# Kernel tuning notes

Hardware: AMD Instinct MI355X
Metric: run time of the kernel (lower is better)

Reference implementation:

```python
import jax, jax.numpy as jnp
import numpy as np

PAD = 1
VOCAB, D, HOPS = 32000, 256, 3

def _gru_dir(x_tbd, h0, Wih, Whh, bih, bhh):
    # x_tbd: [T,B,D]; PyTorch GRU gate math
    def step(h, xt):
        gx = xt @ Wih.T + bih            # [B,3D]
        gh = h @ Whh.T + bhh
        xr, xz, xn = jnp.split(gx, 3, axis=-1)
        hr, hz, hn = jnp.split(gh, 3, axis=-1)
        r = jax.nn.sigmoid(xr + hr)
        z = jax.nn.sigmoid(xz + hz)
        n = jnp.tanh(xn + r * hn)
        h2 = (1.0 - z) * n + z * h
        return h2, h2
    hT, ys = jax.lax.scan(step, h0, x_tbd)
    return ys, hT

def _embed_bag(table, idx):
    # idx: [B,L,M] -> sum over M -> [B,L,D]
    return jnp.take(table, idx, axis=0).sum(axis=2)

def _add_lm(full_mem, kb_len, conv_len, hiddens):
    # full_mem: [B,L,D]; hiddens: [B,T,D]; write hiddens into rows [kb, kb+cl)
    B, L, _ = full_mem.shape
    T = hiddens.shape[1]
    pos = jnp.arange(L)[None, :]                      # [1,L]
    rel = pos - kb_len[:, None]                        # [B,L]
    valid = (rel >= 0) & (rel < conv_len[:, None])
    rel_c = jnp.clip(rel, 0, T - 1)
    gathered = jnp.take_along_axis(hiddens, rel_c[:, :, None], axis=1)  # [B,L,D]
    return full_mem + jnp.where(valid[:, :, None], gathered, 0.0)

def setup_inputs() -> dict:
    key = jax.random.key(0)
    ks = jax.random.split(key, 20)
    B, T, L, M = 32, 128, 512, 4
    conv_seqs = jax.random.randint(ks[0], (B, T, M), 0, VOCAB)
    src_seqs = jax.random.randint(ks[1], (B, L, M), 0, VOCAB)
    kb_len = jnp.full((B,), L - T, dtype=jnp.int32)
    conv_len = jnp.full((B,), T, dtype=jnp.int32)
    def zero_pad(t):
        return t.at[PAD].set(0.0)
    emb_ctx = zero_pad(0.1 * jax.random.normal(ks[2], (VOCAB, D)))
    C_tables = zero_pad(0.1 * jax.random.normal(ks[3], (HOPS + 1, VOCAB, D)).transpose(1, 0, 2)).transpose(1, 0, 2)
    s = 1.0 / np.sqrt(D)
    Wih_f = jax.random.uniform(ks[4], (3 * D, D), minval=-s, maxval=s)
    Whh_f = jax.random.uniform(ks[5], (3 * D, D), minval=-s, maxval=s)
    bih_f = jax.random.uniform(ks[6], (3 * D,), minval=-s, maxval=s)
    bhh_f = jax.random.uniform(ks[7], (3 * D,), minval=-s, maxval=s)
    Wih_b = jax.random.uniform(ks[8], (3 * D, D), minval=-s, maxval=s)
    Whh_b = jax.random.uniform(ks[9], (3 * D, D), minval=-s, maxval=s)
    bih_b = jax.random.uniform(ks[10], (3 * D,), minval=-s, maxval=s)
    bhh_b = jax.random.uniform(ks[11], (3 * D,), minval=-s, maxval=s)
    W_w = jax.random.uniform(ks[12], (D, 2 * D), minval=-s, maxval=s)
    W_b = jax.random.uniform(ks[13], (D,), minval=-s, maxval=s)
    proj_w = jax.random.uniform(ks[14], (D, 2 * D), minval=-s, maxval=s)
    proj_b = jax.random.uniform(ks[15], (D,), minval=-s, maxval=s)
    return dict(conv_seqs=conv_seqs, src_seqs=src_seqs, kb_len=kb_len, conv_len=conv_len,
                emb_ctx=emb_ctx, C_tables=C_tables,
                Wih_f=Wih_f, Whh_f=Whh_f, bih_f=bih_f, bhh_f=bhh_f,
                Wih_b=Wih_b, Whh_b=Whh_b, bih_b=bih_b, bhh_b=bhh_b,
                W_w=W_w, W_b=W_b, proj_w=proj_w, proj_b=proj_b)

def reference(conv_seqs, src_seqs, kb_len, conv_len, emb_ctx, C_tables,
              Wih_f, Whh_f, bih_f, bhh_f, Wih_b, Whh_b, bih_b, bhh_b,
              W_w, W_b, proj_w, proj_b):
    B = conv_seqs.shape[0]
    # ContextRNN (dropout is identity at eval)
    emb = _embed_bag(emb_ctx, conv_seqs)               # [B,T,D]
    x = emb.transpose(1, 0, 2)                          # [T,B,D]
    h0 = jnp.zeros((B, D), emb.dtype)
    ys_f, hT_f = _gru_dir(x, h0, Wih_f, Whh_f, bih_f, bhh_f)
    ys_b, hT_b = _gru_dir(x[::-1], h0, Wih_b, Whh_b, bih_b, bhh_b)
    outputs = jnp.concatenate([ys_f, ys_b[::-1]], axis=-1).transpose(1, 0, 2)  # [B,T,2D]
    hidden = jnp.concatenate([hT_f, hT_b], axis=-1) @ W_w.T + W_b              # [B,D]
    rnn_out = outputs @ W_w.T + W_b                                            # [B,T,D]
    # ExternalKnowledge encode
    u = hidden
    prob_logit = None
    embed_C = None
    for hop in range(HOPS):
        embed_A = _add_lm(_embed_bag(C_tables[hop], src_seqs), kb_len, conv_len, rnn_out)
        embed_C = _add_lm(_embed_bag(C_tables[hop + 1], src_seqs), kb_len, conv_len, rnn_out)
        prob_logit = jnp.einsum('bld,bd->bl', embed_A, u)
        prob = jax.nn.softmax(prob_logit, axis=1)
        o_k = jnp.einsum('bld,bl->bd', embed_C, prob)
        u = u + o_k
    global_pointer = jax.nn.sigmoid(prob_logit)
    encoded = jax.nn.relu(jnp.concatenate([hidden, u], axis=-1) @ proj_w.T + proj_b)[None]
    return global_pointer, encoded
```

## Files before the change

kernel.cpp:

```cpp
#include <hip/hip_runtime.h>

typedef _Float16 f16;
typedef _Float16 f16x8 __attribute__((ext_vector_type(8)));
typedef _Float16 f16x4 __attribute__((ext_vector_type(4)));
typedef float    f32x4 __attribute__((ext_vector_type(4)));


__device__ __forceinline__ float frcp(float x){
  float r; asm("v_rcp_f32 %0, %1" : "=v"(r) : "v"(x)); return r;
}
__device__ __forceinline__ float fsig(float x){ return frcp(1.0f + __expf(-x)); }
__device__ __forceinline__ float ftanh(float x){ return 2.0f*frcp(1.0f + __expf(-2.0f*x)) - 1.0f; }

__global__ void k_zero(float* out){
  int i = blockIdx.x*256 + threadIdx.x;
  if (i < 24576) out[i] = 0.f;
}

__global__ void k_cvtall(const float* __restrict__ s0, const float* __restrict__ s1,
                         const float* __restrict__ s2, const float* __restrict__ s3,
                         const float* __restrict__ s4,
                         f16* __restrict__ d0, f16* __restrict__ d1,
                         f16* __restrict__ d2, f16* __restrict__ d3,
                         f16* __restrict__ d4){
  int i = blockIdx.x*256 + threadIdx.x;
  d0[i] = (f16)s0[i];
  d1[i] = (f16)s1[i];
  d2[i] = (f16)s2[i];
  d3[i] = (f16)s3[i];
  if (i < 131072) d4[i] = (f16)s4[i];
}

__global__ void k_embbag(const int* __restrict__ conv, const float* __restrict__ tbl,
                         f16* __restrict__ emb){
  int bt = blockIdx.x, d = threadIdx.x;
  const int* ix = conv + (size_t)bt*4;
  float s = 0.f;
#pragma unroll
  for (int m = 0; m < 4; ++m) s += tbl[(size_t)ix[m]*256 + d];
  emb[(size_t)bt*256 + d] = (f16)s;
}

__global__ __launch_bounds__(256) void k_gx(const f16* __restrict__ emb,
                                            const f16* __restrict__ W16,
                                            const float* __restrict__ bih,
                                            const float* __restrict__ bhh,
                                            f16* __restrict__ gx, int rev){
  int lane = threadIdx.x & 63, wv = threadIdx.x >> 6;
  int l16 = lane & 15, l4 = lane >> 4;
  int mrow = blockIdx.x*64 + wv*16;
  int m = mrow + l16;
  int t = m >> 5, b = m & 31;
  int tsrc = rev ? (127 - t) : t;
  const f16* arow = emb + (size_t)(b*128 + tsrc)*256;
  f16x8 af[8];
#pragma unroll
  for (int kt = 0; kt < 8; ++kt) af[kt] = *(const f16x8*)(arow + kt*32 + l4*8);

  for (int nt = 0; nt < 48; ++nt){
    int n = nt*16 + l16;
    const f16* brow = W16 + (size_t)n*256;
    f32x4 acc = {0.f,0.f,0.f,0.f};
#pragma unroll
    for (int kt = 0; kt < 8; ++kt){
      f16x8 bf = *(const f16x8*)(brow + kt*32 + l4*8);
      acc = __builtin_amdgcn_mfma_f32_16x16x32_f16(af[kt], bf, acc, 0, 0, 0);
    }
    float bias = bih[n] + (n < 512 ? bhh[n] : 0.f);
#pragma unroll
    for (int r = 0; r < 4; ++r){
      int m2 = mrow + l4*4 + r;
      gx[(size_t)m2*768 + n] = (f16)(acc[r] + bias);
    }
  }
}

__global__ __launch_bounds__(512, 1) void k_gru(const f16* __restrict__ gx_f,
                                                const f16* __restrict__ gx_b,
                                                const f16* __restrict__ whhf16,
                                                const f16* __restrict__ whhb16,
                                                const float* __restrict__ bhh_f,
                                                const float* __restrict__ bhh_b,
                                                f16* __restrict__ Abuf){
  int dir = blockIdx.x >> 1, grp = blockIdx.x & 1, b0 = grp*16;
  const f16*   gx  = dir ? gx_b   : gx_f;
  const f16*   Whh = dir ? whhb16 : whhf16;
  const float* bhh = dir ? bhh_b  : bhh_f;

  int tid = threadIdx.x, lane = tid & 63, wv = tid >> 6;
  int l16 = lane & 15, l4 = lane >> 4;

  __shared__ __align__(16) f16   a16[2][16][264];
  __shared__ __align__(16) float bhnL[256];
  for (int i = tid; i < (16*264*2)/4; i += 512) ((unsigned*)&a16[0][0][0])[i] = 0u;
  if (tid < 256) bhnL[tid] = bhh[512 + tid];

  f16x8 aW[2][3][8];
#pragma unroll
  for (int q = 0; q < 2; ++q){
    int Q = 2*wv + q;
#pragma unroll
    for (int g = 0; g < 3; ++g){
      const f16* wrow = Whh + (size_t)(g*256 + Q*16 + l16)*256;
#pragma unroll
      for (int kt = 0; kt < 8; ++kt) aW[q][g][kt] = *(const f16x8*)(wrow + kt*32 + l4*8);
    }
  }

  const f16* gp = gx + (size_t)(b0 + l16)*768;
  f16* ap  = Abuf + (size_t)(b0 + l16)*128*512 + dir*256
           + (size_t)(dir ? 127 : 0)*512;
  int  astep = dir ? -512 : 512;
  f16* app = ap;

  const int d00 = (2*wv    )*16 + l4*4;
  const int d01 = (2*wv + 1)*16 + l4*4;

  f16x4 pend[2];
  pend[0] = (f16x4){(f16)0.f,(f16)0.f,(f16)0.f,(f16)0.f};
  pend[1] = (f16x4){(f16)0.f,(f16)0.f,(f16)0.f,(f16)0.f};

  __syncthreads();

#pragma unroll 1
  for (int t = 0; t < 128; ++t){
    if (t){
      *(f16x4*)(app + d00) = pend[0];
      *(f16x4*)(app + d01) = pend[1];
    }

    f16x4 xg[2][3];
#pragma unroll
    for (int q = 0; q < 2; ++q)
#pragma unroll
      for (int g = 0; g < 3; ++g)
        xg[q][g] = *(const f16x4*)(gp + g*256 + (2*wv+q)*16 + l4*4);

    const f16* rb = &a16[t & 1][l16][l4*8];

    f32x4 accr[2], accz[2];
#pragma unroll
    for (int q = 0; q < 2; ++q){ accr[q] = (f32x4){0.f,0.f,0.f,0.f};
                                 accz[q] = (f32x4){0.f,0.f,0.f,0.f}; }
#pragma unroll
    for (int kt = 0; kt < 8; ++kt){
      f16x8 bf = *(const f16x8*)(rb + kt*32);
#pragma unroll
      for (int q = 0; q < 2; ++q){
        accr[q] = __builtin_amdgcn_mfma_f32_16x16x32_f16(aW[q][0][kt], bf, accr[q], 0, 0, 0);
        accz[q] = __builtin_amdgcn_mfma_f32_16x16x32_f16(aW[q][1][kt], bf, accz[q], 0, 0, 0);
      }
    }

    f32x4 accn[2];
#pragma unroll
    for (int q = 0; q < 2; ++q) accn[q] = (f32x4){0.f,0.f,0.f,0.f};
#pragma unroll
    for (int kt = 0; kt < 8; ++kt){
      f16x8 bf = *(const f16x8*)(rb + kt*32);
#pragma unroll
      for (int q = 0; q < 2; ++q)
        accn[q] = __builtin_amdgcn_mfma_f32_16x16x32_f16(aW[q][2][kt], bf, accn[q], 0, 0, 0);
    }

    float rr[2][4], zz[2][4];
#pragma unroll
    for (int q = 0; q < 2; ++q)
#pragma unroll
      for (int r = 0; r < 4; ++r){
        rr[q][r] = fsig((float)xg[q][0][r] + accr[q][r]);
        zz[q][r] = fsig((float)xg[q][1][r] + accz[q][r]);
      }

    int nxt = (t & 1) ^ 1;
#pragma unroll
    for (int q = 0; q < 2; ++q){
      int d0 = (2*wv+q)*16 + l4*4;
      float4 bh4 = *(const float4*)(&bhnL[d0]);
      f16x4 hold = pend[q];
      f16x4 o4;
#pragma unroll
      for (int r = 0; r < 4; ++r){
        float bh = (r==0)?bh4.x:(r==1)?bh4.y:(r==2)?bh4.z:bh4.w;
        float nn = ftanh((float)xg[q][2][r] + rr[q][r]*(accn[q][r] + bh));
        float h2 = nn + zz[q][r]*((float)hold[r] - nn);
        o4[r] = (f16)h2;
      }
      *(f16x4*)(&a16[nxt][l16][d0]) = o4;
      pend[q] = o4;
    }
    app = ap; ap += astep;
    gp += 24576;
    __syncthreads();
  }
  *(f16x4*)(app + d00) = pend[0];
  *(f16x4*)(app + d01) = pend[1];
}

__global__ __launch_bounds__(256) void k_rnnout(const f16* __restrict__ Abuf,
                                                const f16* __restrict__ Ww16,
                                                const float* __restrict__ Wb,
                                                float* __restrict__ rnn){
  int lane = threadIdx.x & 63, wv = threadIdx.x >> 6;
  int l16 = lane & 15, l4 = lane >> 4;
  int mrow = blockIdx.x*64 + wv*16;
  const f16* arow = Abuf + (size_t)(mrow + l16)*512;
  f16x8 af[16];
#pragma unroll
  for (int kt = 0; kt < 16; ++kt) af[kt] = *(const f16x8*)(arow + kt*32 + l4*8);
  for (int nt = 0; nt < 16; ++nt){
    int n = nt*16 + l16;
    const f16* brow = Ww16 + (size_t)n*512;
    f32x4 acc = {0.f,0.f,0.f,0.f};
#pragma unroll
    for (int kt = 0; kt < 16; ++kt){
      f16x8 bf = *(const f16x8*)(brow + kt*32 + l4*8);
      acc = __builtin_amdgcn_mfma_f32_16x16x32_f16(af[kt], bf, acc, 0, 0, 0);
    }
    float bias = Wb[n];
#pragma unroll
    for (int r = 0; r < 4; ++r)
      rnn[(size_t)(mrow + l4*4 + r)*256 + n] = acc[r] + bias;
  }
}

__global__ __launch_bounds__(256) void k_hidden(const f16* __restrict__ Abuf,
                                                const f16* __restrict__ Ww16,
                                                const float* __restrict__ Wb,
                                                float* __restrict__ hidden,
                                                float* __restrict__ u){
  int lane = threadIdx.x & 63, wv = threadIdx.x >> 6;
  int l16 = lane & 15, l4 = lane >> 4;
  int mt = wv & 1, nt = blockIdx.x*2 + (wv >> 1);
  int b = mt*16 + l16;
  const f16* rowf = Abuf + ((size_t)b*128 + 127)*512;
  const f16* rowb = Abuf + ((size_t)b*128)*512;
  f16x8 af[16];
#pragma unroll
  for (int kt = 0; kt < 16; ++kt){
    int k = kt*32 + l4*8;
    af[kt] = *(const f16x8*)((k < 256 ? rowf : rowb) + k);
  }
  int n = nt*16 + l16;
  const f16* brow = Ww16 + (size_t)n*512;
  f32x4 acc = {0.f,0.f,0.f,0.f};
#pragma unroll
  for (int kt = 0; kt < 16; ++kt){
    f16x8 bf = *(const f16x8*)(brow + kt*32 + l4*8);
    acc = __builtin_amdgcn_mfma_f32_16x16x32_f16(af[kt], bf, acc, 0, 0, 0);
  }
  float bias = Wb[n];
#pragma unroll
  for (int r = 0; r < 4; ++r){
    int bo = mt*16 + l4*4 + r;
    float v = acc[r] + bias;
    hidden[(size_t)bo*256 + n] = v;
    u[(size_t)bo*256 + n] = v;
  }
}

__global__ __launch_bounds__(256) void k_logits(const int* __restrict__ src,
                                                const int* __restrict__ kbl,
                                                const int* __restrict__ cvl,
                                                const float* __restrict__ tblA,
                                                const float* __restrict__ rnn,
                                                const float* __restrict__ u,
                                                float* __restrict__ logits){
  int b = blockIdx.x >> 5, chunk = blockIdx.x & 31;
  int lane = threadIdx.x & 63, wv = threadIdx.x >> 6;
  int kb = kbl[b], cl = cvl[b];
  float4 uv = *(const float4*)(u + b*256 + lane*4);
#pragma unroll
  for (int i = 0; i < 4; ++i){
    int l = chunk*16 + wv*4 + i;
    const int* sp = src + ((size_t)b*512 + l)*4;
    float b0 = 0.f, b1 = 0.f, b2 = 0.f, b3 = 0.f;
#pragma unroll
    for (int m = 0; m < 4; ++m){
      float4 wq = *(const float4*)(tblA + (size_t)sp[m]*256 + lane*4);
      b0 += wq.x; b1 += wq.y; b2 += wq.z; b3 += wq.w;
    }
    int rel = l - kb;
    if (rel >= 0 && rel < cl){
      int rc = rel < 127 ? rel : 127;
      float4 rv = *(const float4*)(rnn + ((size_t)b*128 + rc)*256 + lane*4);
      b0 += rv.x; b1 += rv.y; b2 += rv.z; b3 += rv.w;
    }
    float p = b0*uv.x + b1*uv.y + b2*uv.z + b3*uv.w;
#pragma unroll
    for (int off = 32; off >= 1; off >>= 1) p += __shfl_down(p, off);
    if (lane == 0) logits[(size_t)b*512 + l] = p;
  }
}

__global__ __launch_bounds__(256) void k_okv(const int* __restrict__ src,
                                             const int* __restrict__ kbl,
                                             const int* __restrict__ cvl,
                                             const float* __restrict__ tblC,
                                             const float* __restrict__ rnn,
                                             const float* __restrict__ logits,
                                             float* __restrict__ u,
                                             float* __restrict__ gp_out, int write_gp){
  int b = blockIdx.x >> 3, c = blockIdx.x & 7;
  int d = threadIdx.x, lane = d & 63, wv = d >> 6;
  __shared__ float red[4];
  __shared__ float bc;
  __shared__ float pr[512];
  __shared__ int   sidx[256];

  float v0 = logits[(size_t)b*512 + d];
  float v1 = logits[(size_t)b*512 + 256 + d];
  float m = fmaxf(v0, v1);
#pragma unroll
  for (int off = 32; off >= 1; off >>= 1) m = fmaxf(m, __shfl_down(m, off));
  if (lane == 0) red[wv] = m;
  __syncthreads();
  if (d == 0) bc = fmaxf(fmaxf(red[0], red[1]), fmaxf(red[2], red[3]));
  __syncthreads();
  float mx = bc;
  float e0 = __expf(v0 - mx), e1 = __expf(v1 - mx);
  float s = e0 + e1;
#pragma unroll
  for (int off = 32; off >= 1; off >>= 1) s += __shfl_down(s, off);
  __syncthreads();
  if (lane == 0) red[wv] = s;
  __syncthreads();
  if (d == 0) bc = red[0] + red[1] + red[2] + red[3];
  __syncthreads();
  float inv = 1.0f/bc;
  pr[d] = e0*inv; pr[256 + d] = e1*inv;
  sidx[d] = src[(size_t)b*2048 + c*256 + d];
  if (write_gp && c == 0){
    gp_out[(size_t)b*512 + d]       = fsig(v0);
    gp_out[(size_t)b*512 + 256 + d] = fsig(v1);
  }
  __syncthreads();

  int kb = kbl[b], cl = cvl[b];
  float acc = 0.f;
  for (int l = 0; l < 64; ++l){
    const int* sp = sidx + l*4;
    float bag = tblC[(size_t)sp[0]*256 + d] + tblC[(size_t)sp[1]*256 + d]
              + tblC[(size_t)sp[2]*256 + d] + tblC[(size_t)sp[3]*256 + d];
    int rel = (c*64 + l) - kb;
    if (rel >= 0 && rel < cl){
      int rc = rel < 127 ? rel : 127;
      bag += rnn[((size_t)b*128 + rc)*256 + d];
    }
    acc += pr[c*64 + l] * bag;
  }
  atomicAdd(&u[(size_t)b*256 + d], acc);
}

__global__ void k_encoded(const float* __restrict__ hidden, const float* __restrict__ u,
                          const float* __restrict__ pw, const float* __restrict__ pb,
                          float* __restrict__ out){
  int b = blockIdx.x, d = threadIdx.x;
  const float* w = pw + (size_t)d*512;
  float s = pb[d];
  for (int k = 0; k < 256; ++k) s += hidden[b*256 + k] * w[k];
  for (int k = 0; k < 256; ++k) s += u[b*256 + k]      * w[256 + k];
  out[(size_t)b*256 + d] = fmaxf(s, 0.f);
}

extern "C" void kernel_launch(void* const* d_in, const int* in_sizes, int n_in,
                              void* d_out, int out_size, void* d_ws, size_t ws_size,
                              hipStream_t stream){
  (void)in_sizes; (void)n_in; (void)out_size;
  float* out = (float*)d_out;

  const size_t WS_NEEDED = 25034752;
  if (ws_size < WS_NEEDED){
    k_zero<<<96, 256, 0, stream>>>(out);
    return;
  }

  const int* conv  = (const int*)d_in[0];
  const int* src   = (const int*)d_in[1];
  const int* kbl   = (const int*)d_in[2];
  const int* cvl   = (const int*)d_in[3];
  const float* emb_ctx = (const float*)d_in[4];
  const float* Ct      = (const float*)d_in[5];
  const float* Wih_f = (const float*)d_in[6];
  const float* Whh_f = (const float*)d_in[7];
  const float* bih_f = (const float*)d_in[8];
  const float* bhh_f = (const float*)d_in[9];
  const float* Wih_b = (const float*)d_in[10];
  const float* Whh_b = (const float*)d_in[11];
  const float* bih_b = (const float*)d_in[12];
  const float* bhh_b = (const float*)d_in[13];
  const float* Ww = (const float*)d_in[14];
  const float* Wb = (const float*)d_in[15];
  const float* pw = (const float*)d_in[16];
  const float* pb = (const float*)d_in[17];

  char* ws = (char*)d_ws;
  f16*   emb    = (f16*)(ws);
  f16*   gx_f   = (f16*)(ws + 2097152);
  f16*   gx_b   = (f16*)(ws + 8388608);
  f16*   Abuf   = (f16*)(ws + 14680064);
  float* rnn    = (float*)(ws + 18874368);
  float* hidden = (float*)(ws + 23068672);
  float* u      = (float*)(ws + 23101440);
  float* logits = (float*)(ws + 23134208);
  f16*   wihf16 = (f16*)(ws + 23199744);
  f16*   wihb16 = (f16*)(ws + 23592960);
  f16*   whhf16 = (f16*)(ws + 23986176);
  f16*   whhb16 = (f16*)(ws + 24379392);
  f16*   ww16   = (f16*)(ws + 24772608);

  k_cvtall<<<768, 256, 0, stream>>>(Wih_f, Wih_b, Whh_f, Whh_b, Ww,
                                    wihf16, wihb16, whhf16, whhb16, ww16);
  k_embbag<<<4096, 256, 0, stream>>>(conv, emb_ctx, emb);
  k_gx<<<64, 256, 0, stream>>>(emb, wihf16, bih_f, bhh_f, gx_f, 0);
  k_gx<<<64, 256, 0, stream>>>(emb, wihb16, bih_b, bhh_b, gx_b, 1);
  k_gru<<<4, 512, 0, stream>>>(gx_f, gx_b, whhf16, whhb16, bhh_f, bhh_b, Abuf);
  k_rnnout<<<64, 256, 0, stream>>>(Abuf, ww16, Wb, rnn);
  k_hidden<<<8, 256, 0, stream>>>(Abuf, ww16, Wb, hidden, u);

  for (int hop = 0; hop < 3; ++hop){
    const float* tA = Ct + (size_t)hop     * 32000 * 256;
    const float* tC = Ct + (size_t)(hop+1) * 32000 * 256;
    k_logits<<<1024, 256, 0, stream>>>(src, kbl, cvl, tA, rnn, u, logits);
    k_okv<<<256, 256, 0, stream>>>(src, kbl, cvl, tC, rnn, logits, u,
                                   out, hop == 2 ? 1 : 0);
  }
  k_encoded<<<32, 256, 0, stream>>>(hidden, u, pw, pb, out + 16384);
}
```

Baseline: 916.2 us.

## Split GRU recurrence across 16 waves, one hidden tile per wave

The recurrent GRU kernel now launches 1024 threads per block instead of 512, and each wave owns a single 16-column hidden tile instead of two. This halves the serial MFMA chain and gate math per wave on each time step, shortening the latency-bound critical path of the 128-step recurrence. In exchange the per-step block barrier covers twice as many waves, and per-wave weight registers drop from 48 to 24 vectors. The gx loads for the n gate are also deferred until after the r/z MFMAs.

```diff
diff --git a/kernel.cpp b/kernel.cpp
--- a/kernel.cpp
+++ b/kernel.cpp
@@ -75,13 +75,13 @@
   }
 }
 
-__global__ __launch_bounds__(512, 1) void k_gru(const f16* __restrict__ gx_f,
-                                                const f16* __restrict__ gx_b,
-                                                const f16* __restrict__ whhf16,
-                                                const f16* __restrict__ whhb16,
-                                                const float* __restrict__ bhh_f,
-                                                const float* __restrict__ bhh_b,
-                                                f16* __restrict__ Abuf){
+__global__ __launch_bounds__(1024, 1) void k_gru(const f16* __restrict__ gx_f,
+                                                 const f16* __restrict__ gx_b,
+                                                 const f16* __restrict__ whhf16,
+                                                 const f16* __restrict__ whhb16,
+                                                 const float* __restrict__ bhh_f,
+                                                 const float* __restrict__ bhh_b,
+                                                 f16* __restrict__ Abuf){
   int dir = blockIdx.x >> 1, grp = blockIdx.x & 1, b0 = grp*16;
   const f16*   gx  = dir ? gx_b   : gx_f;
   const f16*   Whh = dir ? whhb16 : whhf16;
@@ -92,109 +92,80 @@
 
   __shared__ __align__(16) f16   a16[2][16][264];
   __shared__ __align__(16) float bhnL[256];
-  for (int i = tid; i < (16*264*2)/4; i += 512) ((unsigned*)&a16[0][0][0])[i] = 0u;
+  for (int i = tid; i < (16*264*2)/4; i += 1024) ((unsigned*)&a16[0][0][0])[i] = 0u;
   if (tid < 256) bhnL[tid] = bhh[512 + tid];
 
-  f16x8 aW[2][3][8];
-#pragma unroll
-  for (int q = 0; q < 2; ++q){
-    int Q = 2*wv + q;
-#pragma unroll
-    for (int g = 0; g < 3; ++g){
-      const f16* wrow = Whh + (size_t)(g*256 + Q*16 + l16)*256;
-#pragma unroll
-      for (int kt = 0; kt < 8; ++kt) aW[q][g][kt] = *(const f16x8*)(wrow + kt*32 + l4*8);
-    }
-  }
-
+  const int Q = wv;
+  f16x8 aW[3][8];
+#pragma unroll
+  for (int g = 0; g < 3; ++g){
+    const f16* wrow = Whh + (size_t)(g*256 + Q*16 + l16)*256;
+#pragma unroll
+    for (int kt = 0; kt < 8; ++kt) aW[g][kt] = *(const f16x8*)(wrow + kt*32 + l4*8);
+  }
+
+  const int d0 = Q*16 + l4*4;
   const f16* gp = gx + (size_t)(b0 + l16)*768;
   f16* ap  = Abuf + (size_t)(b0 + l16)*128*512 + dir*256
            + (size_t)(dir ? 127 : 0)*512;
   int  astep = dir ? -512 : 512;
   f16* app = ap;
 
-  const int d00 = (2*wv    )*16 + l4*4;
-  const int d01 = (2*wv + 1)*16 + l4*4;
-
-  f16x4 pend[2];
-  pend[0] = (f16x4){(f16)0.f,(f16)0.f,(f16)0.f,(f16)0.f};
-  pend[1] = (f16x4){(f16)0.f,(f16)0.f,(f16)0.f,(f16)0.f};
+  f16x4 pend = (f16x4){(f16)0.f,(f16)0.f,(f16)0.f,(f16)0.f};
 
   __syncthreads();
 
 #pragma unroll 1
   for (int t = 0; t < 128; ++t){
-    if (t){
-      *(f16x4*)(app + d00) = pend[0];
-      *(f16x4*)(app + d01) = pend[1];
-    }
-
-    f16x4 xg[2][3];
-#pragma unroll
-    for (int q = 0; q < 2; ++q)
-#pragma unroll
-      for (int g = 0; g < 3; ++g)
-        xg[q][g] = *(const f16x4*)(gp + g*256 + (2*wv+q)*16 + l4*4);
+    if (t) *(f16x4*)(app + d0) = pend;
+
+    f16x4 xgr = *(const f16x4*)(gp + 0*256 + d0);
+    f16x4 xgz = *(const f16x4*)(gp + 1*256 + d0);
 
     const f16* rb = &a16[t & 1][l16][l4*8];
 
-    f32x4 accr[2], accz[2];
-#pragma unroll
-    for (int q = 0; q < 2; ++q){ accr[q] = (f32x4){0.f,0.f,0.f,0.f};
-                                 accz[q] = (f32x4){0.f,0.f,0.f,0.f}; }
+    f32x4 accr = {0.f,0.f,0.f,0.f}, accz = {0.f,0.f,0.f,0.f};
 #pragma unroll
     for (int kt = 0; kt < 8; ++kt){
       f16x8 bf = *(const f16x8*)(rb + kt*32);
-#pragma unroll
-      for (int q = 0; q < 2; ++q){
-        accr[q] = __builtin_amdgcn_mfma_f32_16x16x32_f16(aW[q][0][kt], bf, accr[q], 0, 0, 0);
-        accz[q] = __builtin_amdgcn_mfma_f32_16x16x32_f16(aW[q][1][kt], bf, accz[q], 0, 0, 0);
-      }
-    }
-
-    f32x4 accn[2];
-#pragma unroll
-    for (int q = 0; q < 2; ++q) accn[q] = (f32x4){0.f,0.f,0.f,0.f};
+      accr = __builtin_amdgcn_mfma_f32_16x16x32_f16(aW[0][kt], bf, accr, 0, 0, 0);
+      accz = __builtin_amdgcn_mfma_f32_16x16x32_f16(aW[1][kt], bf, accz, 0, 0, 0);
+    }
+
+    f16x4 xgn = *(const f16x4*)(gp + 2*256 + d0);
+    f32x4 accn = {0.f,0.f,0.f,0.f};
 #pragma unroll
     for (int kt = 0; kt < 8; ++kt){
       f16x8 bf = *(const f16x8*)(rb + kt*32);
-#pragma unroll
-      for (int q = 0; q < 2; ++q)
-        accn[q] = __builtin_amdgcn_mfma_f32_16x16x32_f16(aW[q][2][kt], bf, accn[q], 0, 0, 0);
-    }
-
-    float rr[2][4], zz[2][4];
-#pragma unroll
-    for (int q = 0; q < 2; ++q)
-#pragma unroll
-      for (int r = 0; r < 4; ++r){
-        rr[q][r] = fsig((float)xg[q][0][r] + accr[q][r]);
-        zz[q][r] = fsig((float)xg[q][1][r] + accz[q][r]);
-      }
+      accn = __builtin_amdgcn_mfma_f32_16x16x32_f16(aW[2][kt], bf, accn, 0, 0, 0);
+    }
+
+    float rr[4], zz[4];
+#pragma unroll
+    for (int r = 0; r < 4; ++r){
+      rr[r] = fsig((float)xgr[r] + accr[r]);
+      zz[r] = fsig((float)xgz[r] + accz[r]);
+    }
 
     int nxt = (t & 1) ^ 1;
-#pragma unroll
-    for (int q = 0; q < 2; ++q){
-      int d0 = (2*wv+q)*16 + l4*4;
-      float4 bh4 = *(const float4*)(&bhnL[d0]);
-      f16x4 hold = pend[q];
-      f16x4 o4;
-#pragma unroll
-      for (int r = 0; r < 4; ++r){
-        float bh = (r==0)?bh4.x:(r==1)?bh4.y:(r==2)?bh4.z:bh4.w;
-        float nn = ftanh((float)xg[q][2][r] + rr[q][r]*(accn[q][r] + bh));
-        float h2 = nn + zz[q][r]*((float)hold[r] - nn);
-        o4[r] = (f16)h2;
-      }
-      *(f16x4*)(&a16[nxt][l16][d0]) = o4;
-      pend[q] = o4;
-    }
+    float4 bh4 = *(const float4*)(&bhnL[d0]);
+    f16x4 hold = pend;
+    f16x4 o4;
+#pragma unroll
+    for (int r = 0; r < 4; ++r){
+      float bh = (r==0)?bh4.x:(r==1)?bh4.y:(r==2)?bh4.z:bh4.w;
+      float nn = ftanh((float)xgn[r] + rr[r]*(accn[r] + bh));
+      float h2 = nn + zz[r]*((float)hold[r] - nn);
+      o4[r] = (f16)h2;
+    }
+    *(f16x4*)(&a16[nxt][l16][d0]) = o4;
+    pend = o4;
+
     app = ap; ap += astep;
     gp += 24576;
     __syncthreads();
   }
-  *(f16x4*)(app + d00) = pend[0];
-  *(f16x4*)(app + d01) = pend[1];
+  *(f16x4*)(app + d0) = pend;
 }
 
 __global__ __launch_bounds__(256) void k_rnnout(const f16* __restrict__ Abuf,
@@ -414,7 +385,7 @@
   k_embbag<<<4096, 256, 0, stream>>>(conv, emb_ctx, emb);
   k_gx<<<64, 256, 0, stream>>>(emb, wihf16, bih_f, bhh_f, gx_f, 0);
   k_gx<<<64, 256, 0, stream>>>(emb, wihb16, bih_b, bhh_b, gx_b, 1);
-  k_gru<<<4, 512, 0, stream>>>(gx_f, gx_b, whhf16, whhb16, bhh_f, bhh_b, Abuf);
+  k_gru<<<4, 1024, 0, stream>>>(gx_f, gx_b, whhf16, whhb16, bhh_f, bhh_b, Abuf);
   k_rnnout<<<64, 256, 0, stream>>>(Abuf, ww16, Wb, rnn);
   k_hidden<<<8, 256, 0, stream>>>(Abuf, ww16, Wb, hidden, u);
 
```

Measured after the change: 941.6 us. 2.8% more time.

## Split GRU recurrence across two cooperating blocks with global-memory flag exchange

Applied to the files above, without the earlier changes.

Adds a k_gru_duo kernel that splits each (direction, batch-group) GRU recurrence across two workgroups, each computing half the hidden units. After every timestep the two halves swap their half of the hidden state through global memory, using per-step release/acquire flags tagged with an epoch counter that k_cvtall increments. This halves per-CU MFMA and register work on the serial critical path but adds a cross-CU handshake each step. It relies on the workspace being large enough and on both partner blocks being co-resident, otherwise it falls back to the old kernel.

```diff
diff --git a/kernel.cpp b/kernel.cpp
--- a/kernel.cpp
+++ b/kernel.cpp
@@ -4,6 +4,7 @@
 typedef _Float16 f16x8 __attribute__((ext_vector_type(8)));
 typedef _Float16 f16x4 __attribute__((ext_vector_type(4)));
 typedef float    f32x4 __attribute__((ext_vector_type(4)));
+typedef unsigned long long u64;
 
 
 __device__ __forceinline__ float frcp(float x){
@@ -22,8 +23,9 @@
                          const float* __restrict__ s4,
                          f16* __restrict__ d0, f16* __restrict__ d1,
                          f16* __restrict__ d2, f16* __restrict__ d3,
-                         f16* __restrict__ d4){
+                         f16* __restrict__ d4, unsigned* epoch){
   int i = blockIdx.x*256 + threadIdx.x;
+  if (epoch && i == 0) atomicAdd(epoch, 1u);
   d0[i] = (f16)s0[i];
   d1[i] = (f16)s1[i];
   d2[i] = (f16)s2[i];
@@ -75,13 +77,13 @@
   }
 }
 
-__global__ __launch_bounds__(512, 1) void k_gru(const f16* __restrict__ gx_f,
-                                                const f16* __restrict__ gx_b,
-                                                const f16* __restrict__ whhf16,
-                                                const f16* __restrict__ whhb16,
-                                                const float* __restrict__ bhh_f,
-                                                const float* __restrict__ bhh_b,
-                                                f16* __restrict__ Abuf){
+__global__ __launch_bounds__(512, 1) void k_gru_solo(const f16* __restrict__ gx_f,
+                                                     const f16* __restrict__ gx_b,
+                                                     const f16* __restrict__ whhf16,
+                                                     const f16* __restrict__ whhb16,
+                                                     const float* __restrict__ bhh_f,
+                                                     const float* __restrict__ bhh_b,
+                                                     f16* __restrict__ Abuf){
   int dir = blockIdx.x >> 1, grp = blockIdx.x & 1, b0 = grp*16;
   const f16*   gx  = dir ? gx_b   : gx_f;
   const f16*   Whh = dir ? whhb16 : whhf16;
@@ -108,8 +110,7 @@
   }
 
   const f16* gp = gx + (size_t)(b0 + l16)*768;
-  f16* ap  = Abuf + (size_t)(b0 + l16)*128*512 + dir*256
-           + (size_t)(dir ? 127 : 0)*512;
+  f16* ap  = Abuf + (size_t)(b0 + l16)*128*512 + dir*256 + (size_t)(dir ? 127 : 0)*512;
   int  astep = dir ? -512 : 512;
   f16* app = ap;
 
@@ -128,7 +129,6 @@
       *(f16x4*)(app + d00) = pend[0];
       *(f16x4*)(app + d01) = pend[1];
     }
-
     f16x4 xg[2][3];
 #pragma unroll
     for (int q = 0; q < 2; ++q)
@@ -151,7 +151,6 @@
         accz[q] = __builtin_amdgcn_mfma_f32_16x16x32_f16(aW[q][1][kt], bf, accz[q], 0, 0, 0);
       }
     }
-
     f32x4 accn[2];
 #pragma unroll
     for (int q = 0; q < 2; ++q) accn[q] = (f32x4){0.f,0.f,0.f,0.f};
@@ -162,7 +161,6 @@
       for (int q = 0; q < 2; ++q)
         accn[q] = __builtin_amdgcn_mfma_f32_16x16x32_f16(aW[q][2][kt], bf, accn[q], 0, 0, 0);
     }
-
     float rr[2][4], zz[2][4];
 #pragma unroll
     for (int q = 0; q < 2; ++q)
@@ -171,7 +169,6 @@
         rr[q][r] = fsig((float)xg[q][0][r] + accr[q][r]);
         zz[q][r] = fsig((float)xg[q][1][r] + accz[q][r]);
       }
-
     int nxt = (t & 1) ^ 1;
 #pragma unroll
     for (int q = 0; q < 2; ++q){
@@ -195,6 +192,128 @@
   }
   *(f16x4*)(app + d00) = pend[0];
   *(f16x4*)(app + d01) = pend[1];
+}
+
+__global__ __launch_bounds__(512, 1) void k_gru_duo(const f16* __restrict__ gx_f,
+                                                    const f16* __restrict__ gx_b,
+                                                    const f16* __restrict__ whhf16,
+                                                    const f16* __restrict__ whhb16,
+                                                    const float* __restrict__ bhh_f,
+                                                    const float* __restrict__ bhh_b,
+                                                    f16* __restrict__ Abuf,
+                                                    char* __restrict__ ext){
+  int bid = blockIdx.x;
+  int dir = bid >> 2, grp = (bid >> 1) & 1, half = bid & 1;
+  int b0 = grp*16;
+  const f16*   gx  = dir ? gx_b   : gx_f;
+  const f16*   Whh = dir ? whhb16 : whhf16;
+  const float* bhh = dir ? bhh_b  : bhh_f;
+
+  int tid = threadIdx.x, lane = tid & 63, wv = tid >> 6;
+  int l16 = lane & 15, l4 = lane >> 4;
+
+  __shared__ __align__(16) f16   a16[2][16][264];
+  __shared__ __align__(16) float bhnL[256];
+  for (int i = tid; i < (16*264*2)/4; i += 512) ((unsigned*)&a16[0][0][0])[i] = 0u;
+  if (tid < 256) bhnL[tid] = bhh[512 + tid];
+
+  int pair = dir*2 + grp;
+  char*     hx_mine    = ext + (size_t)((pair*2 + half      )*2)*4096;
+  char*     hx_partner = ext + (size_t)((pair*2 + (half^1))*2)*4096;
+  unsigned* flags_mine    = (unsigned*)(ext + 131072) + (pair*2 + half      )*128;
+  unsigned* flags_partner = (unsigned*)(ext + 131072) + (pair*2 + (half^1))*128;
+  unsigned epoch = __hip_atomic_load((unsigned*)(ext + 135168),
+                                     __ATOMIC_RELAXED, __HIP_MEMORY_SCOPE_AGENT);
+
+  const int Qg = half*8 + wv;
+  const int d0 = Qg*16 + l4*4;
+  f16x8 aW[3][8];
+#pragma unroll
+  for (int g = 0; g < 3; ++g){
+    const f16* wrow = Whh + (size_t)(g*256 + Qg*16 + l16)*256;
+#pragma unroll
+    for (int kt = 0; kt < 8; ++kt) aW[g][kt] = *(const f16x8*)(wrow + kt*32 + l4*8);
+  }
+
+  const f16* gp = gx + (size_t)(b0 + l16)*768;
+  f16* ap  = Abuf + (size_t)(b0 + l16)*128*512 + dir*256 + (size_t)(dir ? 127 : 0)*512;
+  int  astep = dir ? -512 : 512;
+  f16* app = ap;
+
+  const int myoff = l16*256 + wv*32 + l4*8;
+  const int cb = tid >> 5;
+  const int cc = (tid & 31) * 4;
+  const int poff = (half^1)*128;
+
+  f16x4 pend = (f16x4){(f16)0.f,(f16)0.f,(f16)0.f,(f16)0.f};
+
+  __syncthreads();
+
+#pragma unroll 1
+  for (int t = 0; t < 128; ++t){
+    if (t) *(f16x4*)(app + d0) = pend;
+
+    const f16* rb = &a16[t & 1][l16][l4*8];
+    f16x8 bf[8];
+#pragma unroll
+    for (int kt = 0; kt < 8; ++kt) bf[kt] = *(const f16x8*)(rb + kt*32);
+
+    f16x4 xgr = *(const f16x4*)(gp + 0*256 + d0);
+    f16x4 xgz = *(const f16x4*)(gp + 1*256 + d0);
+    f16x4 xgn = *(const f16x4*)(gp + 2*256 + d0);
+
+    f32x4 accr = {0.f,0.f,0.f,0.f}, accz = {0.f,0.f,0.f,0.f};
+#pragma unroll
+    for (int kt = 0; kt < 8; ++kt){
+      accr = __builtin_amdgcn_mfma_f32_16x16x32_f16(aW[0][kt], bf[kt], accr, 0, 0, 0);
+      accz = __builtin_amdgcn_mfma_f32_16x16x32_f16(aW[1][kt], bf[kt], accz, 0, 0, 0);
+    }
+    f32x4 accn = {0.f,0.f,0.f,0.f};
+#pragma unroll
+    for (int kt = 0; kt < 8; ++kt)
+      accn = __builtin_amdgcn_mfma_f32_16x16x32_f16(aW[2][kt], bf[kt], accn, 0, 0, 0);
+
+    float rr[4], zz[4];
+#pragma unroll
+    for (int r = 0; r < 4; ++r){
+      rr[r] = fsig((float)xgr[r] + accr[r]);
+      zz[r] = fsig((float)xgz[r] + accz[r]);
+    }
+
+    int nxt = (t & 1) ^ 1;
+    float4 bh4 = *(const float4*)(&bhnL[d0]);
+    f16x4 hold = pend;
+    f16x4 o4;
+#pragma unroll
+    for (int r = 0; r < 4; ++r){
+      float bh = (r==0)?bh4.x:(r==1)?bh4.y:(r==2)?bh4.z:bh4.w;
+      float nn = ftanh((float)xgn[r] + rr[r]*(accn[r] + bh));
+      float h2 = nn + zz[r]*((float)hold[r] - nn);
+      o4[r] = (f16)h2;
+    }
+    *(f16x4*)(&a16[nxt][l16][d0]) = o4;
+    pend = o4;
+    app = ap; ap += astep;
+    gp += 24576;
+
+    if (t < 127){
+      __hip_atomic_store((u64*)(hx_mine + (size_t)(t&1)*4096 + myoff),
+                         __builtin_bit_cast(u64, o4),
+                         __ATOMIC_RELAXED, __HIP_MEMORY_SCOPE_AGENT);
+      __syncthreads();
+      if (tid == 0)
+        __hip_atomic_store(&flags_mine[t], epoch,
+                           __ATOMIC_RELEASE, __HIP_MEMORY_SCOPE_AGENT);
+      while (__hip_atomic_load(&flags_partner[t],
+                               __ATOMIC_ACQUIRE, __HIP_MEMORY_SCOPE_AGENT) != epoch)
+        __builtin_amdgcn_s_sleep(2);
+      u64 v = __hip_atomic_load((u64*)(hx_partner + (size_t)(t&1)*4096 + cb*256 + cc*2),
+                                __ATOMIC_RELAXED, __HIP_MEMORY_SCOPE_AGENT);
+      *(u64*)((char*)&a16[nxt][cb][0] + (size_t)(poff + cc)*2) = v;
+      __syncthreads();
+    }
+  }
+  *(f16x4*)(app + d0) = pend;
 }
 
 __global__ __launch_bounds__(256) void k_rnnout(const f16* __restrict__ Abuf,
@@ -370,10 +489,13 @@
   float* out = (float*)d_out;
 
   const size_t WS_NEEDED = 25034752;
+  const size_t EXT_OFF   = 25034752;
+  const size_t WS_BIG    = EXT_OFF + 135176;
   if (ws_size < WS_NEEDED){
     k_zero<<<96, 256, 0, stream>>>(out);
     return;
   }
+  bool big = ws_size >= WS_BIG;
 
   const int* conv  = (const int*)d_in[0];
   const int* src   = (const int*)d_in[1];
@@ -408,13 +530,18 @@
   f16*   whhf16 = (f16*)(ws + 23986176);
   f16*   whhb16 = (f16*)(ws + 24379392);
   f16*   ww16   = (f16*)(ws + 24772608);
+  char*  ext    = ws + EXT_OFF;
+  unsigned* epoch = big ? (unsigned*)(ext + 135168) : nullptr;
 
   k_cvtall<<<768, 256, 0, stream>>>(Wih_f, Wih_b, Whh_f, Whh_b, Ww,
-                                    wihf16, wihb16, whhf16, whhb16, ww16);
+                                    wihf16, wihb16, whhf16, whhb16, ww16, epoch);
   k_embbag<<<4096, 256, 0, stream>>>(conv, emb_ctx, emb);
   k_gx<<<64, 256, 0, stream>>>(emb, wihf16, bih_f, bhh_f, gx_f, 0);
   k_gx<<<64, 256, 0, stream>>>(emb, wihb16, bih_b, bhh_b, gx_b, 1);
-  k_gru<<<4, 512, 0, stream>>>(gx_f, gx_b, whhf16, whhb16, bhh_f, bhh_b, Abuf);
+  if (big)
+    k_gru_duo<<<8, 512, 0, stream>>>(gx_f, gx_b, whhf16, whhb16, bhh_f, bhh_b, Abuf, ext);
+  else
+    k_gru_solo<<<4, 512, 0, stream>>>(gx_f, gx_b, whhf16, whhb16, bhh_f, bhh_b, Abuf);
   k_rnnout<<<64, 256, 0, stream>>>(Abuf, ww16, Wb, rnn);
   k_hidden<<<8, 256, 0, stream>>>(Abuf, ww16, Wb, hidden, u);
 
```

After: 1.072 ms. +17.0%, slower.

## Reuse hop's embed_C bag as next hop's embed_A via f16 buffer

Applied to the files above, without the earlier changes.

Each hop's k_okv now writes its computed memory bag (table gather plus rnn row) to a workspace buffer in f16. The next hop's k_logits reads that buffer instead of re-gathering four embedding rows, since embed_C of one hop equals embed_A of the next. k_okv's grid is also doubled, with half as many rows per block, for more parallelism. The cost is extra bag writes, f16 rounding of the logits input, and more atomics on u.

```diff
diff --git a/kernel.cpp b/kernel.cpp
--- a/kernel.cpp
+++ b/kernel.cpp
@@ -108,8 +108,7 @@
   }
 
   const f16* gp = gx + (size_t)(b0 + l16)*768;
-  f16* ap  = Abuf + (size_t)(b0 + l16)*128*512 + dir*256
-           + (size_t)(dir ? 127 : 0)*512;
+  f16* ap  = Abuf + (size_t)(b0 + l16)*128*512 + dir*256 + (size_t)(dir ? 127 : 0)*512;
   int  astep = dir ? -512 : 512;
   f16* app = ap;
 
@@ -128,7 +127,6 @@
       *(f16x4*)(app + d00) = pend[0];
       *(f16x4*)(app + d01) = pend[1];
     }
-
     f16x4 xg[2][3];
 #pragma unroll
     for (int q = 0; q < 2; ++q)
@@ -151,7 +149,6 @@
         accz[q] = __builtin_amdgcn_mfma_f32_16x16x32_f16(aW[q][1][kt], bf, accz[q], 0, 0, 0);
       }
     }
-
     f32x4 accn[2];
 #pragma unroll
     for (int q = 0; q < 2; ++q) accn[q] = (f32x4){0.f,0.f,0.f,0.f};
@@ -162,7 +159,6 @@
       for (int q = 0; q < 2; ++q)
         accn[q] = __builtin_amdgcn_mfma_f32_16x16x32_f16(aW[q][2][kt], bf, accn[q], 0, 0, 0);
     }
-
     float rr[2][4], zz[2][4];
 #pragma unroll
     for (int q = 0; q < 2; ++q)
@@ -171,7 +167,6 @@
         rr[q][r] = fsig((float)xg[q][0][r] + accr[q][r]);
         zz[q][r] = fsig((float)xg[q][1][r] + accz[q][r]);
       }
-
     int nxt = (t & 1) ^ 1;
 #pragma unroll
     for (int q = 0; q < 2; ++q){
@@ -265,11 +260,25 @@
                                                 const float* __restrict__ tblA,
                                                 const float* __restrict__ rnn,
                                                 const float* __restrict__ u,
-                                                float* __restrict__ logits){
+                                                float* __restrict__ logits,
+                                                const f16* __restrict__ bagin){
   int b = blockIdx.x >> 5, chunk = blockIdx.x & 31;
   int lane = threadIdx.x & 63, wv = threadIdx.x >> 6;
+  float4 uv = *(const float4*)(u + b*256 + lane*4);
+  if (bagin){
+#pragma unroll
+    for (int i = 0; i < 4; ++i){
+      int l = chunk*16 + wv*4 + i;
+      f16x4 bv = *(const f16x4*)(bagin + ((size_t)b*512 + l)*256 + lane*4);
+      float p = (float)bv[0]*uv.x + (float)bv[1]*uv.y
+              + (float)bv[2]*uv.z + (float)bv[3]*uv.w;
+#pragma unroll
+      for (int off = 32; off >= 1; off >>= 1) p += __shfl_down(p, off);
+      if (lane == 0) logits[(size_t)b*512 + l] = p;
+    }
+    return;
+  }
   int kb = kbl[b], cl = cvl[b];
-  float4 uv = *(const float4*)(u + b*256 + lane*4);
 #pragma unroll
   for (int i = 0; i < 4; ++i){
     int l = chunk*16 + wv*4 + i;
@@ -300,13 +309,14 @@
                                              const float* __restrict__ rnn,
                                              const float* __restrict__ logits,
                                              float* __restrict__ u,
-                                             float* __restrict__ gp_out, int write_gp){
-  int b = blockIdx.x >> 3, c = blockIdx.x & 7;
+                                             float* __restrict__ gp_out, int write_gp,
+                                             f16* __restrict__ bagout){
+  int b = blockIdx.x >> 4, c = blockIdx.x & 15;
   int d = threadIdx.x, lane = d & 63, wv = d >> 6;
   __shared__ float red[4];
   __shared__ float bc;
   __shared__ float pr[512];
-  __shared__ int   sidx[256];
+  __shared__ int   sidx[128];
 
   float v0 = logits[(size_t)b*512 + d];
   float v1 = logits[(size_t)b*512 + 256 + d];
@@ -329,7 +339,7 @@
   __syncthreads();
   float inv = 1.0f/bc;
   pr[d] = e0*inv; pr[256 + d] = e1*inv;
-  sidx[d] = src[(size_t)b*2048 + c*256 + d];
+  if (d < 128) sidx[d] = src[(size_t)b*2048 + c*128 + d];
   if (write_gp && c == 0){
     gp_out[(size_t)b*512 + d]       = fsig(v0);
     gp_out[(size_t)b*512 + 256 + d] = fsig(v1);
@@ -338,16 +348,17 @@
 
   int kb = kbl[b], cl = cvl[b];
   float acc = 0.f;
-  for (int l = 0; l < 64; ++l){
+  for (int l = 0; l < 32; ++l){
     const int* sp = sidx + l*4;
     float bag = tblC[(size_t)sp[0]*256 + d] + tblC[(size_t)sp[1]*256 + d]
               + tblC[(size_t)sp[2]*256 + d] + tblC[(size_t)sp[3]*256 + d];
-    int rel = (c*64 + l) - kb;
+    int rel = (c*32 + l) - kb;
     if (rel >= 0 && rel < cl){
       int rc = rel < 127 ? rel : 127;
       bag += rnn[((size_t)b*128 + rc)*256 + d];
     }
-    acc += pr[c*64 + l] * bag;
+    if (bagout) bagout[((size_t)b*512 + c*32 + l)*256 + d] = (f16)bag;
+    acc += pr[c*32 + l] * bag;
   }
   atomicAdd(&u[(size_t)b*256 + d], acc);
 }
@@ -408,6 +419,7 @@
   f16*   whhf16 = (f16*)(ws + 23986176);
   f16*   whhb16 = (f16*)(ws + 24379392);
   f16*   ww16   = (f16*)(ws + 24772608);
+  f16*   bagbuf = (f16*)(ws + 2097152);
 
   k_cvtall<<<768, 256, 0, stream>>>(Wih_f, Wih_b, Whh_f, Whh_b, Ww,
                                     wihf16, wihb16, whhf16, whhb16, ww16);
@@ -421,9 +433,11 @@
   for (int hop = 0; hop < 3; ++hop){
     const float* tA = Ct + (size_t)hop     * 32000 * 256;
     const float* tC = Ct + (size_t)(hop+1) * 32000 * 256;
-    k_logits<<<1024, 256, 0, stream>>>(src, kbl, cvl, tA, rnn, u, logits);
-    k_okv<<<256, 256, 0, stream>>>(src, kbl, cvl, tC, rnn, logits, u,
-                                   out, hop == 2 ? 1 : 0);
+    k_logits<<<1024, 256, 0, stream>>>(src, kbl, cvl, tA, rnn, u, logits,
+                                       hop ? bagbuf : (const f16*)nullptr);
+    k_okv<<<512, 256, 0, stream>>>(src, kbl, cvl, tC, rnn, logits, u,
+                                   out, hop == 2 ? 1 : 0,
+                                   hop < 2 ? bagbuf : (f16*)nullptr);
   }
   k_encoded<<<32, 256, 0, stream>>>(hidden, u, pw, pb, out + 16384);
 }
```

Measured after the change: 848.5 us. -7.4%, faster.
